# Kernel tuning notes

Measured on AMD Instinct MI355X. Metric: run time of the kernel, lower is better.

Reference implementation:

```python
import jax, jax.numpy as jnp
import numpy as np

B, N, H, D = 1024, 128, 128, 8  # batch, num_nodes (= num variables), hidden, diffusion size


def setup_inputs() -> dict:
    key = jax.random.key(0)
    ks = jax.random.split(key, 7)
    return {
        "x": jax.random.normal(ks[0], (B, N), dtype=jnp.float32),
        "f_weight": jax.random.normal(ks[1], (N, N, H), dtype=jnp.float32) * 0.1,
        "g_weight": jax.random.normal(ks[2], (N, N, H, D), dtype=jnp.float32) * 0.1,
        "Wf": jax.random.normal(ks[3], (N, H), dtype=jnp.float32) * (1.0 / np.sqrt(H)),
        "bf": jax.random.normal(ks[4], (N,), dtype=jnp.float32) * 0.01,
        "Wg": jax.random.normal(ks[5], (N, H), dtype=jnp.float32) * (1.0 / np.sqrt(H)),
        "bg": jax.random.normal(ks[6], (N,), dtype=jnp.float32) * 0.01,
    }


def reference(x, f_weight, g_weight, Wf, bf, Wg, bg):
    # Drift f: per node i, temp_i = x @ f_weight[i]  -> [B,H]; out_i = fc_i(elu(temp_i)) -> [B,1]
    # Batched over nodes as a single einsum instead of the original Python loop.
    temp_f = jnp.einsum('bn,inh->bih', x, f_weight)              # [B,N,H]
    f_out = jnp.einsum('bih,ih->bi', jax.nn.elu(temp_f), Wf) + bf  # [B,N]

    # Diffusion g: per node i, temp_i = x @ g_weight[i] -> [B,H,D]; fc_i applied over H per diffusion channel.
    temp_g = jnp.einsum('bn,inhd->bihd', x, g_weight)            # [B,N,H,D]
    g_out = jnp.einsum('bihd,ih->bid', jax.nn.elu(temp_g), Wg) + bg[None, :, None]  # [B,N,D]
    return f_out, g_out
```

## Files before the change

### kernel.cpp

```cpp
#include <hip/hip_runtime.h>
#include <hip/hip_bf16.h>


typedef unsigned short u16;
typedef __attribute__((ext_vector_type(8))) short bf16x8;
typedef __attribute__((ext_vector_type(4))) float f32x4;

#define LOG2E 1.4426950408889634f
#define LN2   0.6931471805599453f

__device__ __forceinline__ uint32_t pk2(float a, float b) {
    union { __hip_bfloat162 h2; uint32_t u; } c;
    c.h2 = __float22bfloat162_rn(make_float2(a, b));
    return c.u;
}
__device__ __forceinline__ float elu_acc(float u, float wv, float p) {
    float m = fmaxf(u, 0.f);
    float e = __builtin_amdgcn_exp2f(fminf(u, 0.f));
    return fmaf(fmaf(m, LN2, e), wv, p);
}

__global__ __launch_bounds__(256, 4) void sde_fused(
    const float* __restrict__ x, const float* __restrict__ fw, const float* __restrict__ gw,
    const float* __restrict__ Wf, const float* __restrict__ bfp,
    const float* __restrict__ Wg, const float* __restrict__ bgp,
    float* __restrict__ out)
{
    __shared__ u16 wst[2][64 * 128];
    __shared__ float wgs[128];
    __shared__ float wfs[128];

    const int t = threadIdx.x, bx = blockIdx.x;
    const int i    = bx & 127;
    const int b0   = (bx >> 7) << 7;
    const int w    = t >> 6;
    const int lane = t & 63;
    const int l15  = lane & 15;
    const int quad = lane >> 4;
    const int l31  = lane & 31;
    const int jj   = lane >> 5;
    const int c0   = l31 * 2;
    const int sw   = (l15 >> 1) & 7;

    if (t < 128) { wgs[t] = Wg[i * 128 + t]; wfs[t] = Wf[i * 128 + t]; }

    bf16x8 afr[2][4];
    #pragma unroll
    for (int rs = 0; rs < 2; ++rs) {
        const float* xr = x + (size_t)(b0 + w * 32 + rs * 16 + l15) * 128 + quad * 8;
        #pragma unroll
        for (int kk = 0; kk < 4; ++kk) {
            float4 v0 = *(const float4*)(xr + kk * 32);
            float4 v1 = *(const float4*)(xr + kk * 32 + 4);
            union { uint32_t u[4]; bf16x8 v; } r;
            r.u[0] = pk2(v0.x * LOG2E, v0.y * LOG2E);
            r.u[1] = pk2(v0.z * LOG2E, v0.w * LOG2E);
            r.u[2] = pk2(v1.x * LOG2E, v1.y * LOG2E);
            r.u[3] = pk2(v1.z * LOG2E, v1.w * LOG2E);
            afr[rs][kk] = r.v;
        }
    }

    const float* gwi = gw + (size_t)i * 131072;
    const float* fwi = fw + (size_t)i * 16384;

    float2 vr[8];
    auto load_half = [&](int ct, int half) {
        const float* src; int rstride;
        if (ct < 16) { src = gwi + ct * 64;        rstride = 1024; }
        else         { src = fwi + (ct - 16) * 64; rstride = 128;  }
        const int j = half * 8 + w * 2 + jj;
        const float* s2 = src + (size_t)(8 * j) * rstride + c0;
        #pragma unroll
        for (int r = 0; r < 8; ++r) vr[r] = *(const float2*)(s2 + (size_t)r * rstride);
    };
    auto write_half = [&](int p, int half) {
        const int j = half * 8 + w * 2 + jj;
        const int slot = (j ^ (l31 & 7)) << 3;
        union { uint32_t u[4]; bf16x8 v; } rr;
        rr.u[0] = pk2(vr[0].x, vr[1].x); rr.u[1] = pk2(vr[2].x, vr[3].x);
        rr.u[2] = pk2(vr[4].x, vr[5].x); rr.u[3] = pk2(vr[6].x, vr[7].x);
        *(bf16x8*)&wst[p][c0 * 128 + slot] = rr.v;
        rr.u[0] = pk2(vr[0].y, vr[1].y); rr.u[1] = pk2(vr[2].y, vr[3].y);
        rr.u[2] = pk2(vr[4].y, vr[5].y); rr.u[3] = pk2(vr[6].y, vr[7].y);
        *(bf16x8*)&wst[p][(c0 + 1) * 128 + slot] = rr.v;
    };

    load_half(16, 0); write_half(0, 0);
    load_half(16, 1); write_half(0, 1);
    __syncthreads();

    float racc[8];
    #pragma unroll
    for (int q = 0; q < 8; ++q) racc[q] = 0.f;
    const float bfv = bfp[i], bgv = bgp[i];

    int p = 0;
    for (int idx = 0; idx < 18; ++idx) {
        const int ct  = (idx < 2) ? 16 + idx : idx - 2;
        const bool pre = idx < 17;
        const int ctn = (idx == 0) ? 17 : idx - 1;

        f32x4 acc[2][4];
        #pragma unroll
        for (int rs = 0; rs < 2; ++rs)
            #pragma unroll
            for (int cs = 0; cs < 4; ++cs)
                acc[rs][cs] = (f32x4){0.f, 0.f, 0.f, 0.f};

        if (pre) load_half(ctn, 0);

        #pragma unroll
        for (int kk = 0; kk < 2; ++kk) {
            const int co = ((kk * 4 + quad) ^ sw) << 3;
            bf16x8 bv[4];
            #pragma unroll
            for (int cs = 0; cs < 4; ++cs)
                bv[cs] = *(const bf16x8*)&wst[p][(cs * 16 + l15) * 128 + co];
            #pragma unroll
            for (int cs = 0; cs < 4; ++cs) {
                acc[0][cs] = __builtin_amdgcn_mfma_f32_16x16x32_bf16(afr[0][kk], bv[cs], acc[0][cs], 0, 0, 0);
                acc[1][cs] = __builtin_amdgcn_mfma_f32_16x16x32_bf16(afr[1][kk], bv[cs], acc[1][cs], 0, 0, 0);
            }
        }

        if (pre) { write_half(p ^ 1, 0); load_half(ctn, 1); }

        #pragma unroll
        for (int kk = 2; kk < 4; ++kk) {
            const int co = ((kk * 4 + quad) ^ sw) << 3;
            bf16x8 bv[4];
            #pragma unroll
            for (int cs = 0; cs < 4; ++cs)
                bv[cs] = *(const bf16x8*)&wst[p][(cs * 16 + l15) * 128 + co];
            #pragma unroll
            for (int cs = 0; cs < 4; ++cs) {
                acc[0][cs] = __builtin_amdgcn_mfma_f32_16x16x32_bf16(afr[0][kk], bv[cs], acc[0][cs], 0, 0, 0);
                acc[1][cs] = __builtin_amdgcn_mfma_f32_16x16x32_bf16(afr[1][kk], bv[cs], acc[1][cs], 0, 0, 0);
            }
        }

        if (idx < 2) {
            float wv[4];
            #pragma unroll
            for (int cs = 0; cs < 4; ++cs) wv[cs] = wfs[(ct - 16) * 64 + cs * 16 + l15];
            #pragma unroll
            for (int rs = 0; rs < 2; ++rs)
                #pragma unroll
                for (int rg = 0; rg < 4; ++rg) {
                    float s = racc[rs * 4 + rg];
                    s = elu_acc(acc[rs][0][rg], wv[0], s);
                    s = elu_acc(acc[rs][1][rg], wv[1], s);
                    s = elu_acc(acc[rs][2][rg], wv[2], s);
                    s = elu_acc(acc[rs][3][rg], wv[3], s);
                    racc[rs * 4 + rg] = s;
                }
        } else {
            float wv[4];
            #pragma unroll
            for (int cs = 0; cs < 4; ++cs) wv[cs] = wgs[ct * 8 + cs * 2 + (l15 >> 3)];
            #pragma unroll
            for (int rs = 0; rs < 2; ++rs)
                #pragma unroll
                for (int rg = 0; rg < 4; ++rg) {
                    float s = racc[rs * 4 + rg];
                    s = elu_acc(acc[rs][0][rg], wv[0], s);
                    s = elu_acc(acc[rs][1][rg], wv[1], s);
                    s = elu_acc(acc[rs][2][rg], wv[2], s);
                    s = elu_acc(acc[rs][3][rg], wv[3], s);
                    racc[rs * 4 + rg] = s;
                }
        }

        if (pre) write_half(p ^ 1, 1);

        if (idx == 1) {
            float Sf = 0.f;
            #pragma unroll
            for (int jh = 0; jh < 8; ++jh) Sf += wfs[jh * 16 + l15];
            #pragma unroll
            for (int rs = 0; rs < 2; ++rs)
                #pragma unroll
                for (int rg = 0; rg < 4; ++rg) {
                    float f = racc[rs * 4 + rg] - Sf;
                    f += __shfl_xor(f, 1);
                    f += __shfl_xor(f, 2);
                    f += __shfl_xor(f, 4);
                    f += __shfl_xor(f, 8);
                    if (l15 == 0) {
                        const int row = w * 32 + rs * 16 + quad * 4 + rg;
                        out[(size_t)(b0 + row) * 128 + i] = f + bfv;
                    }
                    racc[rs * 4 + rg] = 0.f;
                }
        }

        if (pre) __syncthreads();
        p ^= 1;
    }

    float Sg = 0.f;
    {
        const int hb = l15 >> 3;
        #pragma unroll 8
        for (int h = 0; h < 128; h += 2) Sg += wgs[h + hb];
    }
    #pragma unroll
    for (int rs = 0; rs < 2; ++rs)
        #pragma unroll
        for (int rg = 0; rg < 4; ++rg) {
            float g = racc[rs * 4 + rg] - Sg;
            g += __shfl_xor(g, 8);
            if (l15 < 8) {
                const int row = w * 32 + rs * 16 + quad * 4 + rg;
                out[(size_t)131072 + ((size_t)(b0 + row) * 128 + i) * 8 + (lane & 7)] = g + bgv;
            }
        }
}

extern "C" void kernel_launch(void* const* d_in, const int* in_sizes, int n_in,
                              void* d_out, int out_size, void* d_ws, size_t ws_size,
                              hipStream_t stream) {
    const float* x  = (const float*)d_in[0];
    const float* fw = (const float*)d_in[1];
    const float* gw = (const float*)d_in[2];
    const float* Wf = (const float*)d_in[3];
    const float* bf = (const float*)d_in[4];
    const float* Wg = (const float*)d_in[5];
    const float* bg = (const float*)d_in[6];
    float* out = (float*)d_out;
    (void)d_ws; (void)ws_size;

    sde_fused<<<1024, 256, 0, stream>>>(x, fw, gw, Wf, bf, Wg, bg, out);
}
```

Measured before the change: 177.5 us.

## Double batch rows per block to halve weight reloads

Each block now covers 256 batch rows instead of 128, so each wave holds four 16-row A fragments and the grid shrinks from 1024 to 512 blocks. Every node's weight slice (f and g) is therefore read from global memory and converted to bf16 in shared memory half as many times, cutting the dominant weight traffic. In exchange it roughly doubles the accumulator and fragment registers and relaxes the occupancy hint to 1-2 waves per EU. Fewer blocks and lower occupancy may leave less latency hiding on a GPU with many CUs.

```diff
diff --git a/kernel.cpp b/kernel.cpp
--- a/kernel.cpp
+++ b/kernel.cpp
@@ -20,7 +20,8 @@
     return fmaf(fmaf(m, LN2, e), wv, p);
 }
 
-__global__ __launch_bounds__(256, 4) void sde_fused(
+__global__ __attribute__((amdgpu_waves_per_eu(1, 2))) __launch_bounds__(256)
+void sde_fused(
     const float* __restrict__ x, const float* __restrict__ fw, const float* __restrict__ gw,
     const float* __restrict__ Wf, const float* __restrict__ bfp,
     const float* __restrict__ Wg, const float* __restrict__ bgp,
@@ -32,7 +33,7 @@
 
     const int t = threadIdx.x, bx = blockIdx.x;
     const int i    = bx & 127;
-    const int b0   = (bx >> 7) << 7;
+    const int b0   = (bx >> 7) << 8;
     const int w    = t >> 6;
     const int lane = t & 63;
     const int l15  = lane & 15;
@@ -44,10 +45,10 @@
 
     if (t < 128) { wgs[t] = Wg[i * 128 + t]; wfs[t] = Wf[i * 128 + t]; }
 
-    bf16x8 afr[2][4];
+    bf16x8 afr[4][4];
     #pragma unroll
-    for (int rs = 0; rs < 2; ++rs) {
-        const float* xr = x + (size_t)(b0 + w * 32 + rs * 16 + l15) * 128 + quad * 8;
+    for (int ms = 0; ms < 4; ++ms) {
+        const float* xr = x + (size_t)(b0 + w * 64 + ms * 16 + l15) * 128 + quad * 8;
         #pragma unroll
         for (int kk = 0; kk < 4; ++kk) {
             float4 v0 = *(const float4*)(xr + kk * 32);
@@ -57,7 +58,7 @@
             r.u[1] = pk2(v0.z * LOG2E, v0.w * LOG2E);
             r.u[2] = pk2(v1.x * LOG2E, v1.y * LOG2E);
             r.u[3] = pk2(v1.z * LOG2E, v1.w * LOG2E);
-            afr[rs][kk] = r.v;
+            afr[ms][kk] = r.v;
         }
     }
 
@@ -90,9 +91,9 @@
     load_half(16, 1); write_half(0, 1);
     __syncthreads();
 
-    float racc[8];
+    float racc[16];
     #pragma unroll
-    for (int q = 0; q < 8; ++q) racc[q] = 0.f;
+    for (int q = 0; q < 16; ++q) racc[q] = 0.f;
     const float bfv = bfp[i], bgv = bgp[i];
 
     int p = 0;
@@ -101,12 +102,12 @@
         const bool pre = idx < 17;
         const int ctn = (idx == 0) ? 17 : idx - 1;
 
-        f32x4 acc[2][4];
-        #pragma unroll
-        for (int rs = 0; rs < 2; ++rs)
+        f32x4 acc[4][4];
+        #pragma unroll
+        for (int ms = 0; ms < 4; ++ms)
             #pragma unroll
             for (int cs = 0; cs < 4; ++cs)
-                acc[rs][cs] = (f32x4){0.f, 0.f, 0.f, 0.f};
+                acc[ms][cs] = (f32x4){0.f, 0.f, 0.f, 0.f};
 
         if (pre) load_half(ctn, 0);
 
@@ -118,10 +119,10 @@
             for (int cs = 0; cs < 4; ++cs)
                 bv[cs] = *(const bf16x8*)&wst[p][(cs * 16 + l15) * 128 + co];
             #pragma unroll
-            for (int cs = 0; cs < 4; ++cs) {
-                acc[0][cs] = __builtin_amdgcn_mfma_f32_16x16x32_bf16(afr[0][kk], bv[cs], acc[0][cs], 0, 0, 0);
-                acc[1][cs] = __builtin_amdgcn_mfma_f32_16x16x32_bf16(afr[1][kk], bv[cs], acc[1][cs], 0, 0, 0);
-            }
+            for (int ms = 0; ms < 4; ++ms)
+                #pragma unroll
+                for (int cs = 0; cs < 4; ++cs)
+                    acc[ms][cs] = __builtin_amdgcn_mfma_f32_16x16x32_bf16(afr[ms][kk], bv[cs], acc[ms][cs], 0, 0, 0);
         }
 
         if (pre) { write_half(p ^ 1, 0); load_half(ctn, 1); }
@@ -134,10 +135,10 @@
             for (int cs = 0; cs < 4; ++cs)
                 bv[cs] = *(const bf16x8*)&wst[p][(cs * 16 + l15) * 128 + co];
             #pragma unroll
-            for (int cs = 0; cs < 4; ++cs) {
-                acc[0][cs] = __builtin_amdgcn_mfma_f32_16x16x32_bf16(afr[0][kk], bv[cs], acc[0][cs], 0, 0, 0);
-                acc[1][cs] = __builtin_amdgcn_mfma_f32_16x16x32_bf16(afr[1][kk], bv[cs], acc[1][cs], 0, 0, 0);
-            }
+            for (int ms = 0; ms < 4; ++ms)
+                #pragma unroll
+                for (int cs = 0; cs < 4; ++cs)
+                    acc[ms][cs] = __builtin_amdgcn_mfma_f32_16x16x32_bf16(afr[ms][kk], bv[cs], acc[ms][cs], 0, 0, 0);
         }
 
         if (idx < 2) {
@@ -145,30 +146,30 @@
             #pragma unroll
             for (int cs = 0; cs < 4; ++cs) wv[cs] = wfs[(ct - 16) * 64 + cs * 16 + l15];
             #pragma unroll
-            for (int rs = 0; rs < 2; ++rs)
+            for (int ms = 0; ms < 4; ++ms)
                 #pragma unroll
                 for (int rg = 0; rg < 4; ++rg) {
-                    float s = racc[rs * 4 + rg];
-                    s = elu_acc(acc[rs][0][rg], wv[0], s);
-                    s = elu_acc(acc[rs][1][rg], wv[1], s);
-                    s = elu_acc(acc[rs][2][rg], wv[2], s);
-                    s = elu_acc(acc[rs][3][rg], wv[3], s);
-                    racc[rs * 4 + rg] = s;
+                    float s = racc[ms * 4 + rg];
+                    s = elu_acc(acc[ms][0][rg], wv[0], s);
+                    s = elu_acc(acc[ms][1][rg], wv[1], s);
+                    s = elu_acc(acc[ms][2][rg], wv[2], s);
+                    s = elu_acc(acc[ms][3][rg], wv[3], s);
+                    racc[ms * 4 + rg] = s;
                 }
         } else {
             float wv[4];
             #pragma unroll
             for (int cs = 0; cs < 4; ++cs) wv[cs] = wgs[ct * 8 + cs * 2 + (l15 >> 3)];
             #pragma unroll
-            for (int rs = 0; rs < 2; ++rs)
+            for (int ms = 0; ms < 4; ++ms)
                 #pragma unroll
                 for (int rg = 0; rg < 4; ++rg) {
-                    float s = racc[rs * 4 + rg];
-                    s = elu_acc(acc[rs][0][rg], wv[0], s);
-                    s = elu_acc(acc[rs][1][rg], wv[1], s);
-                    s = elu_acc(acc[rs][2][rg], wv[2], s);
-                    s = elu_acc(acc[rs][3][rg], wv[3], s);
-                    racc[rs * 4 + rg] = s;
+                    float s = racc[ms * 4 + rg];
+                    s = elu_acc(acc[ms][0][rg], wv[0], s);
+                    s = elu_acc(acc[ms][1][rg], wv[1], s);
+                    s = elu_acc(acc[ms][2][rg], wv[2], s);
+                    s = elu_acc(acc[ms][3][rg], wv[3], s);
+                    racc[ms * 4 + rg] = s;
                 }
         }
 
@@ -179,19 +180,19 @@
             #pragma unroll
             for (int jh = 0; jh < 8; ++jh) Sf += wfs[jh * 16 + l15];
             #pragma unroll
-            for (int rs = 0; rs < 2; ++rs)
+            for (int ms = 0; ms < 4; ++ms)
                 #pragma unroll
                 for (int rg = 0; rg < 4; ++rg) {
-                    float f = racc[rs * 4 + rg] - Sf;
+                    float f = racc[ms * 4 + rg] - Sf;
                     f += __shfl_xor(f, 1);
                     f += __shfl_xor(f, 2);
                     f += __shfl_xor(f, 4);
                     f += __shfl_xor(f, 8);
                     if (l15 == 0) {
-                        const int row = w * 32 + rs * 16 + quad * 4 + rg;
+                        const int row = w * 64 + ms * 16 + quad * 4 + rg;
                         out[(size_t)(b0 + row) * 128 + i] = f + bfv;
                     }
-                    racc[rs * 4 + rg] = 0.f;
+                    racc[ms * 4 + rg] = 0.f;
                 }
         }
 
@@ -206,13 +207,13 @@
         for (int h = 0; h < 128; h += 2) Sg += wgs[h + hb];
     }
     #pragma unroll
-    for (int rs = 0; rs < 2; ++rs)
+    for (int ms = 0; ms < 4; ++ms)
         #pragma unroll
         for (int rg = 0; rg < 4; ++rg) {
-            float g = racc[rs * 4 + rg] - Sg;
+            float g = racc[ms * 4 + rg] - Sg;
             g += __shfl_xor(g, 8);
             if (l15 < 8) {
-                const int row = w * 32 + rs * 16 + quad * 4 + rg;
+                const int row = w * 64 + ms * 16 + quad * 4 + rg;
                 out[(size_t)131072 + ((size_t)(b0 + row) * 128 + i) * 8 + (lane & 7)] = g + bgv;
             }
         }
@@ -231,5 +232,5 @@
     float* out = (float*)d_out;
     (void)d_ws; (void)ws_size;
 
-    sde_fused<<<1024, 256, 0, stream>>>(x, fw, gw, Wf, bf, Wg, bg, out);
-}
+    sde_fused<<<512, 256, 0, stream>>>(x, fw, gw, Wf, bf, Wg, bg, out);
+}
```

After: 194.5 us. +9.6%, slower.

## Split per-node column work across two blocks with workspace merge kernel

Applied to the files above, without the earlier changes.

Halves the column tile width to 32 and doubles the grid, so each (node, batch-tile) pair is handled by two blocks. One block covers the first 18 g-tiles and the other covers the f-tiles plus the remaining g-tiles. Partial g results go to a workspace and a second merge kernel sums them and adds the bias. The intent is more blocks and lower LDS use for better occupancy and load balance, at the cost of extra workspace traffic, a second launch, and reloading x fragments in both blocks.

```diff
diff --git a/kernel.cpp b/kernel.cpp
--- a/kernel.cpp
+++ b/kernel.cpp
@@ -20,27 +20,27 @@
     return fmaf(fmaf(m, LN2, e), wv, p);
 }
 
-__global__ __launch_bounds__(256, 4) void sde_fused(
+__global__ __launch_bounds__(256, 5) void sde_main(
     const float* __restrict__ x, const float* __restrict__ fw, const float* __restrict__ gw,
     const float* __restrict__ Wf, const float* __restrict__ bfp,
-    const float* __restrict__ Wg, const float* __restrict__ bgp,
+    const float* __restrict__ Wg, float* __restrict__ wsp,
     float* __restrict__ out)
 {
-    __shared__ u16 wst[2][64 * 128];
+    __shared__ u16 wst[2][32 * 128];
     __shared__ float wgs[128];
     __shared__ float wfs[128];
 
     const int t = threadIdx.x, bx = blockIdx.x;
     const int i    = bx & 127;
-    const int b0   = (bx >> 7) << 7;
+    const int b0   = ((bx >> 7) & 7) << 7;
+    const int ch   = bx >> 10;
     const int w    = t >> 6;
     const int lane = t & 63;
     const int l15  = lane & 15;
     const int quad = lane >> 4;
-    const int l31  = lane & 31;
-    const int jj   = lane >> 5;
-    const int c0   = l31 * 2;
     const int sw   = (l15 >> 1) & 7;
+    const int tj   = t >> 4;
+    const int c0   = (t & 15) * 2;
 
     if (t < 128) { wgs[t] = Wg[i * 128 + t]; wfs[t] = Wf[i * 128 + t]; }
 
@@ -64,19 +64,19 @@
     const float* gwi = gw + (size_t)i * 131072;
     const float* fwi = fw + (size_t)i * 16384;
 
+    auto tile_of = [&](int idx) { return ch == 0 ? idx : (idx < 4 ? 32 + idx : 14 + idx); };
+
     float2 vr[8];
-    auto load_half = [&](int ct, int half) {
+    auto load_tile = [&](int T) {
         const float* src; int rstride;
-        if (ct < 16) { src = gwi + ct * 64;        rstride = 1024; }
-        else         { src = fwi + (ct - 16) * 64; rstride = 128;  }
-        const int j = half * 8 + w * 2 + jj;
-        const float* s2 = src + (size_t)(8 * j) * rstride + c0;
+        if (T < 32) { src = gwi + T * 32;        rstride = 1024; }
+        else        { src = fwi + (T - 32) * 32; rstride = 128;  }
+        const float* s2 = src + (size_t)(8 * tj) * rstride + c0;
         #pragma unroll
         for (int r = 0; r < 8; ++r) vr[r] = *(const float2*)(s2 + (size_t)r * rstride);
     };
-    auto write_half = [&](int p, int half) {
-        const int j = half * 8 + w * 2 + jj;
-        const int slot = (j ^ (l31 & 7)) << 3;
+    auto write_tile = [&](int p) {
+        const int slot = (tj ^ (t & 7)) << 3;
         union { uint32_t u[4]; bf16x8 v; } rr;
         rr.u[0] = pk2(vr[0].x, vr[1].x); rr.u[1] = pk2(vr[2].x, vr[3].x);
         rr.u[2] = pk2(vr[4].x, vr[5].x); rr.u[3] = pk2(vr[6].x, vr[7].x);
@@ -86,64 +86,47 @@
         *(bf16x8*)&wst[p][(c0 + 1) * 128 + slot] = rr.v;
     };
 
-    load_half(16, 0); write_half(0, 0);
-    load_half(16, 1); write_half(0, 1);
+    load_tile(tile_of(0));
+    write_tile(0);
     __syncthreads();
 
     float racc[8];
     #pragma unroll
     for (int q = 0; q < 8; ++q) racc[q] = 0.f;
-    const float bfv = bfp[i], bgv = bgp[i];
+    const float bfv = bfp[i];
 
     int p = 0;
     for (int idx = 0; idx < 18; ++idx) {
-        const int ct  = (idx < 2) ? 16 + idx : idx - 2;
+        const int T   = tile_of(idx);
         const bool pre = idx < 17;
-        const int ctn = (idx == 0) ? 17 : idx - 1;
-
-        f32x4 acc[2][4];
+
+        if (pre) load_tile(tile_of(idx + 1));
+
+        f32x4 acc[2][2];
         #pragma unroll
         for (int rs = 0; rs < 2; ++rs)
             #pragma unroll
-            for (int cs = 0; cs < 4; ++cs)
+            for (int cs = 0; cs < 2; ++cs)
                 acc[rs][cs] = (f32x4){0.f, 0.f, 0.f, 0.f};
 
-        if (pre) load_half(ctn, 0);
-
-        #pragma unroll
-        for (int kk = 0; kk < 2; ++kk) {
+        #pragma unroll
+        for (int kk = 0; kk < 4; ++kk) {
             const int co = ((kk * 4 + quad) ^ sw) << 3;
-            bf16x8 bv[4];
-            #pragma unroll
-            for (int cs = 0; cs < 4; ++cs)
+            bf16x8 bv[2];
+            #pragma unroll
+            for (int cs = 0; cs < 2; ++cs)
                 bv[cs] = *(const bf16x8*)&wst[p][(cs * 16 + l15) * 128 + co];
             #pragma unroll
-            for (int cs = 0; cs < 4; ++cs) {
-                acc[0][cs] = __builtin_amdgcn_mfma_f32_16x16x32_bf16(afr[0][kk], bv[cs], acc[0][cs], 0, 0, 0);
-                acc[1][cs] = __builtin_amdgcn_mfma_f32_16x16x32_bf16(afr[1][kk], bv[cs], acc[1][cs], 0, 0, 0);
-            }
-        }
-
-        if (pre) { write_half(p ^ 1, 0); load_half(ctn, 1); }
-
-        #pragma unroll
-        for (int kk = 2; kk < 4; ++kk) {
-            const int co = ((kk * 4 + quad) ^ sw) << 3;
-            bf16x8 bv[4];
-            #pragma unroll
-            for (int cs = 0; cs < 4; ++cs)
-                bv[cs] = *(const bf16x8*)&wst[p][(cs * 16 + l15) * 128 + co];
-            #pragma unroll
-            for (int cs = 0; cs < 4; ++cs) {
-                acc[0][cs] = __builtin_amdgcn_mfma_f32_16x16x32_bf16(afr[0][kk], bv[cs], acc[0][cs], 0, 0, 0);
-                acc[1][cs] = __builtin_amdgcn_mfma_f32_16x16x32_bf16(afr[1][kk], bv[cs], acc[1][cs], 0, 0, 0);
-            }
-        }
-
-        if (idx < 2) {
-            float wv[4];
-            #pragma unroll
-            for (int cs = 0; cs < 4; ++cs) wv[cs] = wfs[(ct - 16) * 64 + cs * 16 + l15];
+            for (int rs = 0; rs < 2; ++rs)
+                #pragma unroll
+                for (int cs = 0; cs < 2; ++cs)
+                    acc[rs][cs] = __builtin_amdgcn_mfma_f32_16x16x32_bf16(afr[rs][kk], bv[cs], acc[rs][cs], 0, 0, 0);
+        }
+
+        if (T < 32) {
+            float wv[2];
+            wv[0] = wgs[T * 4 + (l15 >> 3)];
+            wv[1] = wgs[T * 4 + 2 + (l15 >> 3)];
             #pragma unroll
             for (int rs = 0; rs < 2; ++rs)
                 #pragma unroll
@@ -151,14 +134,12 @@
                     float s = racc[rs * 4 + rg];
                     s = elu_acc(acc[rs][0][rg], wv[0], s);
                     s = elu_acc(acc[rs][1][rg], wv[1], s);
-                    s = elu_acc(acc[rs][2][rg], wv[2], s);
-                    s = elu_acc(acc[rs][3][rg], wv[3], s);
                     racc[rs * 4 + rg] = s;
                 }
         } else {
-            float wv[4];
-            #pragma unroll
-            for (int cs = 0; cs < 4; ++cs) wv[cs] = wgs[ct * 8 + cs * 2 + (l15 >> 3)];
+            float wv[2];
+            wv[0] = wfs[(T - 32) * 32 + l15];
+            wv[1] = wfs[(T - 32) * 32 + 16 + l15];
             #pragma unroll
             for (int rs = 0; rs < 2; ++rs)
                 #pragma unroll
@@ -166,15 +147,13 @@
                     float s = racc[rs * 4 + rg];
                     s = elu_acc(acc[rs][0][rg], wv[0], s);
                     s = elu_acc(acc[rs][1][rg], wv[1], s);
-                    s = elu_acc(acc[rs][2][rg], wv[2], s);
-                    s = elu_acc(acc[rs][3][rg], wv[3], s);
                     racc[rs * 4 + rg] = s;
                 }
         }
 
-        if (pre) write_half(p ^ 1, 1);
-
-        if (idx == 1) {
+        if (pre) write_tile(p ^ 1);
+
+        if (ch == 1 && idx == 3) {
             float Sf = 0.f;
             #pragma unroll
             for (int jh = 0; jh < 8; ++jh) Sf += wfs[jh * 16 + l15];
@@ -202,9 +181,10 @@
     float Sg = 0.f;
     {
         const int hb = l15 >> 3;
-        #pragma unroll 8
-        for (int h = 0; h < 128; h += 2) Sg += wgs[h + hb];
+        const int h0 = ch ? 72 : 0, h1 = ch ? 128 : 72;
+        for (int h = h0; h < h1; h += 2) Sg += wgs[h + hb];
     }
+    float* wsc = wsp + (size_t)ch * 1048576;
     #pragma unroll
     for (int rs = 0; rs < 2; ++rs)
         #pragma unroll
@@ -213,9 +193,23 @@
             g += __shfl_xor(g, 8);
             if (l15 < 8) {
                 const int row = w * 32 + rs * 16 + quad * 4 + rg;
-                out[(size_t)131072 + ((size_t)(b0 + row) * 128 + i) * 8 + (lane & 7)] = g + bgv;
+                wsc[((size_t)(b0 + row) * 128 + i) * 8 + (lane & 7)] = g;
             }
         }
+}
+
+__global__ __launch_bounds__(256) void sde_merge(
+    const float* __restrict__ wsp, const float* __restrict__ bgp,
+    float* __restrict__ out)
+{
+    const int tid = blockIdx.x * 256 + threadIdx.x;
+    const float4 a = ((const float4*)wsp)[tid];
+    const float4 b = ((const float4*)(wsp + 1048576))[tid];
+    const float bg = bgp[(tid >> 1) & 127];
+    float4 o;
+    o.x = a.x + b.x + bg; o.y = a.y + b.y + bg;
+    o.z = a.z + b.z + bg; o.w = a.w + b.w + bg;
+    ((float4*)(out + 131072))[tid] = o;
 }
 
 extern "C" void kernel_launch(void* const* d_in, const int* in_sizes, int n_in,
@@ -229,7 +223,8 @@
     const float* Wg = (const float*)d_in[5];
     const float* bg = (const float*)d_in[6];
     float* out = (float*)d_out;
-    (void)d_ws; (void)ws_size;
-
-    sde_fused<<<1024, 256, 0, stream>>>(x, fw, gw, Wf, bf, Wg, bg, out);
-}
+    float* wsp = (float*)d_ws;
+
+    sde_main<<<2048, 256, 0, stream>>>(x, fw, gw, Wf, bf, Wg, wsp, out);
+    sde_merge<<<1024, 256, 0, stream>>>(wsp, bg, out);
+}
```

Result: slower. 185.3 us (+4.4%).
